# Performance work log

Measured on AMD Instinct MI355X. Metric: run time of the kernel, lower is better.

Reference implementation:

```python
import jax, jax.numpy as jnp
import numpy as np

B, C, H, W = 4, 64, 64, 64
CQK = C // 8


def setup_inputs() -> dict:
    key = jax.random.key(0)
    k0, k1, k2, k3, k4 = jax.random.split(key, 5)
    x = jax.random.normal(k0, (B, C, H, W), dtype=jnp.float32)
    # Conv1d kernel_size=1, bias=False -> plain [out, in] matmul weights
    Wq = jax.random.normal(k1, (CQK, C), dtype=jnp.float32) * 0.05
    Wk = jax.random.normal(k2, (CQK, C), dtype=jnp.float32) * 0.05
    Wv = jax.random.normal(k3, (C, C), dtype=jnp.float32) * 0.05
    # torch init is 0; use a nonzero scalar so the attention path is exercised
    gamma = jax.random.uniform(k4, (1,), dtype=jnp.float32)
    return {"x": x, "Wq": Wq, "Wk": Wk, "Wv": Wv, "gamma": gamma}


def reference(x, Wq, Wk, Wv, gamma):
    shape = x.shape                      # [B, C, H, W]
    xf = x.reshape(shape[0], shape[1], -1)  # [B, C, N]
    q = jnp.einsum('oc,bcn->bon', Wq, xf)   # [B, C/8, N]
    k = jnp.einsum('oc,bcn->bon', Wk, xf)   # [B, C/8, N]
    v = jnp.einsum('oc,bcn->bon', Wv, xf)   # [B, C, N]
    # score[b, n, m] = sum_c q[b, c, n] * k[b, c, m]  (no 1/sqrt(d) scale)
    score = jnp.einsum('bcn,bcm->bnm', q, k)  # [B, N, N]
    # unconventional softmax over dim=1 (rows/first N axis, i.e. per-column)
    score = jax.nn.softmax(score, axis=1)
    out = jnp.einsum('bcn,bnm->bcm', v, score)  # [B, C, N]
    attention = gamma * out + xf
    return attention.reshape(shape)
```

## Files before the change

kernel.cpp:

```cpp
#include <hip/hip_runtime.h>

#define BB 4
#define NN 4096

typedef __attribute__((ext_vector_type(8))) short short8v;
typedef __attribute__((ext_vector_type(4))) short short4v;
typedef __attribute__((ext_vector_type(4))) float float4v;

__device__ __forceinline__ unsigned short f2bf_rn(float f) {
    unsigned u = __float_as_uint(f);
    u += 0x7FFFu + ((u >> 16) & 1u);
    return (unsigned short)(u >> 16);
}

__global__ __launch_bounds__(256) void qkv_kernel(
    const float* __restrict__ x,
    const float* __restrict__ Wq, const float* __restrict__ Wk,
    const float* __restrict__ Wv,
    unsigned short* __restrict__ Qt, unsigned short* __restrict__ Kt,
    unsigned short* __restrict__ Vsw)
{
    __shared__ unsigned short xs[64][68];
    __shared__ unsigned short Ot[64][72];

    const int t    = threadIdx.x;
    const int w    = t >> 6;
    const int lane = t & 63;
    const int quad = lane >> 4;
    const int l15  = lane & 15;
    const int b    = blockIdx.y;
    const int n0   = blockIdx.x * 64;

    #pragma unroll
    for (int i = 0; i < 4; ++i) {
        int c  = (t >> 4) + i * 16;
        int n4 = (t & 15) * 4;
        float4 xv = *(const float4*)&x[(size_t)(b * 64 + c) * NN + n0 + n4];
        short4v pk;
        pk[0] = (short)f2bf_rn(xv.x); pk[1] = (short)f2bf_rn(xv.y);
        pk[2] = (short)f2bf_rn(xv.z); pk[3] = (short)f2bf_rn(xv.w);
        *(short4v*)&xs[c][n4] = pk;
    }

    short8v bw[5][2];
    #pragma unroll
    for (int ot = 0; ot < 5; ++ot) {
        int o = ot * 16 + l15;
        const float* base = (o < 8)  ? (Wq + o * 64)
                           : (o < 16) ? (Wk + (o - 8) * 64)
                                      : (Wv + (o - 16) * 64);
        #pragma unroll
        for (int h = 0; h < 2; ++h) {
            float4 u0 = *(const float4*)&base[h * 32 + quad * 8];
            float4 u1 = *(const float4*)&base[h * 32 + quad * 8 + 4];
            short8v f;
            f[0] = (short)f2bf_rn(u0.x); f[1] = (short)f2bf_rn(u0.y);
            f[2] = (short)f2bf_rn(u0.z); f[3] = (short)f2bf_rn(u0.w);
            f[4] = (short)f2bf_rn(u1.x); f[5] = (short)f2bf_rn(u1.y);
            f[6] = (short)f2bf_rn(u1.z); f[7] = (short)f2bf_rn(u1.w);
            bw[ot][h] = f;
        }
    }
    __syncthreads();

    short8v a0, a1;
    {
        unsigned short* p0 = (unsigned short*)&a0;
        unsigned short* p1 = (unsigned short*)&a1;
        const int nn = w * 16 + l15;
        #pragma unroll
        for (int j = 0; j < 8; ++j) {
            p0[j] = xs[quad * 8 + j][nn];
            p1[j] = xs[32 + quad * 8 + j][nn];
        }
    }

    const float4v zacc = {0.f, 0.f, 0.f, 0.f};
    #pragma unroll
    for (int ot = 0; ot < 5; ++ot) {
        float4v d = __builtin_amdgcn_mfma_f32_16x16x32_bf16(a0, bw[ot][0], zacc, 0, 0, 0);
        d = __builtin_amdgcn_mfma_f32_16x16x32_bf16(a1, bw[ot][1], d, 0, 0, 0);
        if (ot == 0) {
            #pragma unroll
            for (int r = 0; r < 4; ++r) {
                unsigned short v = f2bf_rn(d[r]);
                size_t n = (size_t)(n0 + w * 16 + quad * 4 + r);
                if (l15 < 8) Qt[((size_t)b * NN + n) * 8 + l15] = v;
                else         Kt[((size_t)b * NN + n) * 8 + (l15 - 8)] = v;
            }
        } else {
            short4v pk;
            #pragma unroll
            for (int r = 0; r < 4; ++r) pk[r] = (short)f2bf_rn(d[r]);
            *(short4v*)&Ot[(ot - 1) * 16 + l15][w * 16 + quad * 4] = pk;
        }
    }
    __syncthreads();

    {
        int ci = t >> 5, s = t & 31;
        int ct = ci >> 1, nbl = ci & 1;
        size_t nb = (size_t)blockIdx.x * 2 + nbl;
        unsigned short* cb = Vsw + ((size_t)(b * 4 + ct) * 128 + nb) * 512;
        #pragma unroll
        for (int h = 0; h < 2; ++h) {
            int l = s * 2 + h;
            short8v d = *(short8v*)&Ot[ct * 16 + (l & 15)][nbl * 32 + ((l >> 4) << 3)];
            *(short8v*)(cb + l * 8) = d;
        }
    }
}

__global__ __launch_bounds__(256, 4) void attn_kernel(
    const unsigned short* __restrict__ Qt,
    const unsigned short* __restrict__ Kt,
    const unsigned short* __restrict__ Vsw,
    const float* __restrict__ x, const float* __restrict__ gamma,
    float* __restrict__ out)
{
    __shared__ __align__(16) unsigned short Pb[4][16][40];
    __shared__ float Ored[4][64][17];
    __shared__ float Lred[4][16];
    __shared__ float Lf[16];

    const int t    = threadIdx.x;
    const int w    = t >> 6;
    const int lane = t & 63;
    const int quad = lane >> 4;
    const int l15  = lane & 15;
    const int b    = blockIdx.y;
    const int m0   = blockIdx.x * 16;

    const short8v zfrag = {0, 0, 0, 0, 0, 0, 0, 0};
    const float4v zacc  = {0.f, 0.f, 0.f, 0.f};

    short8v bk = zfrag;
    if (quad == 0)
        bk = *(const short8v*)(Kt + (size_t)(b * NN + m0 + l15) * 8);

    float4v acc[4];
    #pragma unroll
    for (int ct = 0; ct < 4; ++ct) acc[ct] = zacc;
    float Lacc = 0.f;

    const unsigned short* qrow = Qt + (size_t)(b * NN + w * 1024 + l15) * 8;
    const unsigned short* vptr = Vsw + ((size_t)b * 4 * 128 + w * 32) * 512 + lane * 8;

    short8v aq0n = zfrag, aq1n = zfrag;
    if (quad == 0) {
        aq0n = *(const short8v*)(qrow);
        aq1n = *(const short8v*)(qrow + 16 * 8);
    }
    short8v av0n = *(const short8v*)(vptr);
    short8v av1n = *(const short8v*)(vptr + 1 * 128 * 512);
    short8v av2n = *(const short8v*)(vptr + 2 * 128 * 512);
    short8v av3n = *(const short8v*)(vptr + 3 * 128 * 512);

    for (int it = 0; it < 32; ++it) {
        short8v aq0 = aq0n, aq1 = aq1n;
        short8v av0 = av0n, av1 = av1n, av2 = av2n, av3 = av3n;

        const int itn = (it + 1) & 31;
        av0n = *(const short8v*)(vptr + itn * 512);
        av1n = *(const short8v*)(vptr + 1 * 128 * 512 + itn * 512);
        av2n = *(const short8v*)(vptr + 2 * 128 * 512 + itn * 512);
        av3n = *(const short8v*)(vptr + 3 * 128 * 512 + itn * 512);
        if (quad == 0) {
            aq0n = *(const short8v*)(qrow + (size_t)(itn * 32) * 8);
            aq1n = *(const short8v*)(qrow + (size_t)(itn * 32 + 16) * 8);
        }

        float4v s0 = __builtin_amdgcn_mfma_f32_16x16x32_bf16(aq0, bk, zacc, 0, 0, 0);
        float4v s1 = __builtin_amdgcn_mfma_f32_16x16x32_bf16(aq1, bk, zacc, 0, 0, 0);

        float p[8];
        #pragma unroll
        for (int j = 0; j < 4; ++j) p[j]     = __expf(s0[j]);
        #pragma unroll
        for (int j = 0; j < 4; ++j) p[4 + j] = __expf(s1[j]);
        float ps = 0.f;
        #pragma unroll
        for (int j = 0; j < 8; ++j) ps += p[j];
        Lacc += ps;

        short4v pk0, pk1;
        #pragma unroll
        for (int j = 0; j < 4; ++j) {
            pk0[j] = (short)f2bf_rn(p[j]);
            pk1[j] = (short)f2bf_rn(p[4 + j]);
        }
        *(short4v*)&Pb[w][l15][quad * 4]      = pk0;
        *(short4v*)&Pb[w][l15][16 + quad * 4] = pk1;

        short8v bp = *(const short8v*)&Pb[w][l15][quad * 8];

        acc[0] = __builtin_amdgcn_mfma_f32_16x16x32_bf16(av0, bp, acc[0], 0, 0, 0);
        acc[1] = __builtin_amdgcn_mfma_f32_16x16x32_bf16(av1, bp, acc[1], 0, 0, 0);
        acc[2] = __builtin_amdgcn_mfma_f32_16x16x32_bf16(av2, bp, acc[2], 0, 0, 0);
        acc[3] = __builtin_amdgcn_mfma_f32_16x16x32_bf16(av3, bp, acc[3], 0, 0, 0);
    }

    Lacc += __shfl_xor(Lacc, 16, 64);
    Lacc += __shfl_xor(Lacc, 32, 64);
    if (lane < 16) Lred[w][lane] = Lacc;

    #pragma unroll
    for (int ct = 0; ct < 4; ++ct)
        #pragma unroll
        for (int r = 0; r < 4; ++r)
            Ored[w][ct * 16 + quad * 4 + r][l15] = acc[ct][r];
    __syncthreads();

    if (t < 16)
        Lf[t] = 1.f / (Lred[0][t] + Lred[1][t] + Lred[2][t] + Lred[3][t]);
    __syncthreads();

    {
        const float gv = gamma[0];
        int c = t >> 2, m4 = (t & 3) * 4;
        float4 o;
        #pragma unroll
        for (int i = 0; i < 4; ++i) {
            float s = Ored[0][c][m4 + i] + Ored[1][c][m4 + i]
                    + Ored[2][c][m4 + i] + Ored[3][c][m4 + i];
            ((float*)&o)[i] = s * Lf[m4 + i];
        }
        size_t gbase = (size_t)(b * 64 + c) * NN + m0 + m4;
        float4 xv = *(const float4*)&x[gbase];
        float4 r;
        r.x = gv * o.x + xv.x; r.y = gv * o.y + xv.y;
        r.z = gv * o.z + xv.z; r.w = gv * o.w + xv.w;
        *(float4*)&out[gbase] = r;
    }
}

extern "C" void kernel_launch(void* const* d_in, const int* in_sizes, int n_in,
                              void* d_out, int out_size, void* d_ws, size_t ws_size,
                              hipStream_t stream) {
    const float* x     = (const float*)d_in[0];
    const float* Wq    = (const float*)d_in[1];
    const float* Wk    = (const float*)d_in[2];
    const float* Wv    = (const float*)d_in[3];
    const float* gamma = (const float*)d_in[4];
    float* out = (float*)d_out;

    unsigned short* ws = (unsigned short*)d_ws;
    unsigned short* Qt  = ws;
    unsigned short* Kt  = Qt + (size_t)BB * NN * 8;
    unsigned short* Vsw = Kt + (size_t)BB * NN * 8;

    qkv_kernel<<<dim3(NN / 64, BB), 256, 0, stream>>>(x, Wq, Wk, Wv, Qt, Kt, Vsw);
    attn_kernel<<<dim3(NN / 16, BB), 256, 0, stream>>>(Qt, Kt, Vsw, x, gamma, out);
}
```

Baseline: 96.47 us.

## Software-pipeline attention loop with double-buffered P and fp32 FMA QKV projection

The attention loop is restructured so the score/exp/pack stage for the next key tile runs while the PV MFMAs consume the previous tile's P from a double-buffered LDS slot, with a prologue and epilogue. The QKV projection kernel replaces its bf16 MFMA path with fp32 FMA over LDS-staged x and transposed weights, and writes Q/K through LDS as coalesced 16-byte rows. The aim is to hide exp and LDS latency behind the matrix ops, and to improve Q/K store coalescing and projection precision. The cost is more LDS use in both kernels and more scalar FMA work in the projection.

New measurement: 97.10 us. About the same (+0.7%).

```diff
diff --git a/kernel.cpp b/kernel.cpp
--- a/kernel.cpp
+++ b/kernel.cpp
@@ -20,82 +20,71 @@
     unsigned short* __restrict__ Qt, unsigned short* __restrict__ Kt,
     unsigned short* __restrict__ Vsw)
 {
-    __shared__ unsigned short xs[64][68];
-    __shared__ unsigned short Ot[64][72];
-
-    const int t    = threadIdx.x;
-    const int w    = t >> 6;
-    const int lane = t & 63;
-    const int quad = lane >> 4;
-    const int l15  = lane & 15;
-    const int b    = blockIdx.y;
-    const int n0   = blockIdx.x * 64;
-
+    __shared__ float xs[64][68];
+    __shared__ float wl[64][81];
+    __shared__ unsigned short Ot[80][72];
+
+    const int t  = threadIdx.x;
+    const int b  = blockIdx.y;
+    const int n0 = blockIdx.x * 64;
+
+    #pragma unroll
+    for (int i = 0; i < 20; ++i) {
+        int idx = t + 256 * i;
+        int r = idx >> 6, c = idx & 63;
+        float w;
+        if (r < 8)       w = Wq[r * 64 + c];
+        else if (r < 16) w = Wk[(r - 8) * 64 + c];
+        else             w = Wv[(r - 16) * 64 + c];
+        wl[c][r] = w;
+    }
     #pragma unroll
     for (int i = 0; i < 4; ++i) {
-        int c  = (t >> 4) + i * 16;
-        int n4 = (t & 15) * 4;
-        float4 xv = *(const float4*)&x[(size_t)(b * 64 + c) * NN + n0 + n4];
+        int idx = t + 256 * i;
+        int c = idx >> 4, n4 = (idx & 15) * 4;
+        *(float4*)&xs[c][n4] = *(const float4*)&x[(size_t)(b * 64 + c) * NN + n0 + n4];
+    }
+    __syncthreads();
+
+    const int n4 = (t & 15) * 4;
+    const int og = t >> 4;
+
+    float acc[5][4];
+    #pragma unroll
+    for (int k = 0; k < 5; ++k)
+        #pragma unroll
+        for (int i = 0; i < 4; ++i) acc[k][i] = 0.f;
+
+    for (int c = 0; c < 64; ++c) {
+        float4 xv = *(const float4*)&xs[c][n4];
+        #pragma unroll
+        for (int k = 0; k < 5; ++k) {
+            float wv = wl[c][og * 5 + k];
+            acc[k][0] += wv * xv.x;
+            acc[k][1] += wv * xv.y;
+            acc[k][2] += wv * xv.z;
+            acc[k][3] += wv * xv.w;
+        }
+    }
+
+    #pragma unroll
+    for (int k = 0; k < 5; ++k) {
         short4v pk;
-        pk[0] = (short)f2bf_rn(xv.x); pk[1] = (short)f2bf_rn(xv.y);
-        pk[2] = (short)f2bf_rn(xv.z); pk[3] = (short)f2bf_rn(xv.w);
-        *(short4v*)&xs[c][n4] = pk;
-    }
-
-    short8v bw[5][2];
-    #pragma unroll
-    for (int ot = 0; ot < 5; ++ot) {
-        int o = ot * 16 + l15;
-        const float* base = (o < 8)  ? (Wq + o * 64)
-                           : (o < 16) ? (Wk + (o - 8) * 64)
-                                      : (Wv + (o - 16) * 64);
-        #pragma unroll
-        for (int h = 0; h < 2; ++h) {
-            float4 u0 = *(const float4*)&base[h * 32 + quad * 8];
-            float4 u1 = *(const float4*)&base[h * 32 + quad * 8 + 4];
-            short8v f;
-            f[0] = (short)f2bf_rn(u0.x); f[1] = (short)f2bf_rn(u0.y);
-            f[2] = (short)f2bf_rn(u0.z); f[3] = (short)f2bf_rn(u0.w);
-            f[4] = (short)f2bf_rn(u1.x); f[5] = (short)f2bf_rn(u1.y);
-            f[6] = (short)f2bf_rn(u1.z); f[7] = (short)f2bf_rn(u1.w);
-            bw[ot][h] = f;
-        }
-    }
-    __syncthreads();
-
-    short8v a0, a1;
-    {
-        unsigned short* p0 = (unsigned short*)&a0;
-        unsigned short* p1 = (unsigned short*)&a1;
-        const int nn = w * 16 + l15;
-        #pragma unroll
-        for (int j = 0; j < 8; ++j) {
-            p0[j] = xs[quad * 8 + j][nn];
-            p1[j] = xs[32 + quad * 8 + j][nn];
-        }
-    }
-
-    const float4v zacc = {0.f, 0.f, 0.f, 0.f};
-    #pragma unroll
-    for (int ot = 0; ot < 5; ++ot) {
-        float4v d = __builtin_amdgcn_mfma_f32_16x16x32_bf16(a0, bw[ot][0], zacc, 0, 0, 0);
-        d = __builtin_amdgcn_mfma_f32_16x16x32_bf16(a1, bw[ot][1], d, 0, 0, 0);
-        if (ot == 0) {
-            #pragma unroll
-            for (int r = 0; r < 4; ++r) {
-                unsigned short v = f2bf_rn(d[r]);
-                size_t n = (size_t)(n0 + w * 16 + quad * 4 + r);
-                if (l15 < 8) Qt[((size_t)b * NN + n) * 8 + l15] = v;
-                else         Kt[((size_t)b * NN + n) * 8 + (l15 - 8)] = v;
-            }
-        } else {
-            short4v pk;
-            #pragma unroll
-            for (int r = 0; r < 4; ++r) pk[r] = (short)f2bf_rn(d[r]);
-            *(short4v*)&Ot[(ot - 1) * 16 + l15][w * 16 + quad * 4] = pk;
-        }
-    }
-    __syncthreads();
+        #pragma unroll
+        for (int i = 0; i < 4; ++i) pk[i] = (short)f2bf_rn(acc[k][i]);
+        *(short4v*)&Ot[og * 5 + k][n4] = pk;
+    }
+    __syncthreads();
+
+    if (t < 128) {
+        int n = t & 63;
+        int rbase = (t < 64) ? 0 : 8;
+        short8v p;
+        #pragma unroll
+        for (int j = 0; j < 8; ++j) p[j] = (short)Ot[rbase + j][n];
+        unsigned short* dst = ((t < 64) ? Qt : Kt) + ((size_t)b * NN + n0 + n) * 8;
+        *(short8v*)dst = p;
+    }
 
     {
         int ci = t >> 5, s = t & 31;
@@ -105,7 +94,7 @@
         #pragma unroll
         for (int h = 0; h < 2; ++h) {
             int l = s * 2 + h;
-            short8v d = *(short8v*)&Ot[ct * 16 + (l & 15)][nbl * 32 + ((l >> 4) << 3)];
+            short8v d = *(short8v*)&Ot[16 + ct * 16 + (l & 15)][nbl * 32 + ((l >> 4) << 3)];
             *(short8v*)(cb + l * 8) = d;
         }
     }
@@ -118,7 +107,7 @@
     const float* __restrict__ x, const float* __restrict__ gamma,
     float* __restrict__ out)
 {
-    __shared__ __align__(16) unsigned short Pb[4][16][40];
+    __shared__ __align__(16) unsigned short Pb[4][2][16][40];
     __shared__ float Ored[4][64][17];
     __shared__ float Lred[4][16];
     __shared__ float Lf[16];
@@ -146,54 +135,77 @@
     const unsigned short* qrow = Qt + (size_t)(b * NN + w * 1024 + l15) * 8;
     const unsigned short* vptr = Vsw + ((size_t)b * 4 * 128 + w * 32) * 512 + lane * 8;
 
-    short8v aq0n = zfrag, aq1n = zfrag;
-    if (quad == 0) {
-        aq0n = *(const short8v*)(qrow);
-        aq1n = *(const short8v*)(qrow + 16 * 8);
-    }
-    short8v av0n = *(const short8v*)(vptr);
-    short8v av1n = *(const short8v*)(vptr + 1 * 128 * 512);
-    short8v av2n = *(const short8v*)(vptr + 2 * 128 * 512);
-    short8v av3n = *(const short8v*)(vptr + 3 * 128 * 512);
-
-    for (int it = 0; it < 32; ++it) {
-        short8v aq0 = aq0n, aq1 = aq1n;
-        short8v av0 = av0n, av1 = av1n, av2 = av2n, av3 = av3n;
-
-        const int itn = (it + 1) & 31;
-        av0n = *(const short8v*)(vptr + itn * 512);
-        av1n = *(const short8v*)(vptr + 1 * 128 * 512 + itn * 512);
-        av2n = *(const short8v*)(vptr + 2 * 128 * 512 + itn * 512);
-        av3n = *(const short8v*)(vptr + 3 * 128 * 512 + itn * 512);
+    short8v av0 = *(const short8v*)(vptr);
+    short8v av1 = *(const short8v*)(vptr + 1 * 128 * 512);
+    short8v av2 = *(const short8v*)(vptr + 2 * 128 * 512);
+    short8v av3 = *(const short8v*)(vptr + 3 * 128 * 512);
+    {
+        short8v aq0 = zfrag, aq1 = zfrag;
         if (quad == 0) {
-            aq0n = *(const short8v*)(qrow + (size_t)(itn * 32) * 8);
-            aq1n = *(const short8v*)(qrow + (size_t)(itn * 32 + 16) * 8);
-        }
-
+            aq0 = *(const short8v*)(qrow);
+            aq1 = *(const short8v*)(qrow + 16 * 8);
+        }
         float4v s0 = __builtin_amdgcn_mfma_f32_16x16x32_bf16(aq0, bk, zacc, 0, 0, 0);
         float4v s1 = __builtin_amdgcn_mfma_f32_16x16x32_bf16(aq1, bk, zacc, 0, 0, 0);
-
         float p[8];
         #pragma unroll
         for (int j = 0; j < 4; ++j) p[j]     = __expf(s0[j]);
         #pragma unroll
         for (int j = 0; j < 4; ++j) p[4 + j] = __expf(s1[j]);
-        float ps = 0.f;
-        #pragma unroll
-        for (int j = 0; j < 8; ++j) ps += p[j];
-        Lacc += ps;
-
+        #pragma unroll
+        for (int j = 0; j < 8; ++j) Lacc += p[j];
         short4v pk0, pk1;
         #pragma unroll
         for (int j = 0; j < 4; ++j) {
             pk0[j] = (short)f2bf_rn(p[j]);
             pk1[j] = (short)f2bf_rn(p[4 + j]);
         }
-        *(short4v*)&Pb[w][l15][quad * 4]      = pk0;
-        *(short4v*)&Pb[w][l15][16 + quad * 4] = pk1;
-
-        short8v bp = *(const short8v*)&Pb[w][l15][quad * 8];
-
+        *(short4v*)&Pb[w][0][l15][quad * 4]      = pk0;
+        *(short4v*)&Pb[w][0][l15][16 + quad * 4] = pk1;
+    }
+
+    for (int it = 0; it < 31; ++it) {
+        const int itn = it + 1;
+
+        short8v avn0 = *(const short8v*)(vptr + itn * 512);
+        short8v avn1 = *(const short8v*)(vptr + 1 * 128 * 512 + itn * 512);
+        short8v avn2 = *(const short8v*)(vptr + 2 * 128 * 512 + itn * 512);
+        short8v avn3 = *(const short8v*)(vptr + 3 * 128 * 512 + itn * 512);
+
+        short8v aq0 = zfrag, aq1 = zfrag;
+        if (quad == 0) {
+            aq0 = *(const short8v*)(qrow + (size_t)(itn * 32) * 8);
+            aq1 = *(const short8v*)(qrow + (size_t)(itn * 32 + 16) * 8);
+        }
+        float4v s0 = __builtin_amdgcn_mfma_f32_16x16x32_bf16(aq0, bk, zacc, 0, 0, 0);
+        float4v s1 = __builtin_amdgcn_mfma_f32_16x16x32_bf16(aq1, bk, zacc, 0, 0, 0);
+        float p[8];
+        #pragma unroll
+        for (int j = 0; j < 4; ++j) p[j]     = __expf(s0[j]);
+        #pragma unroll
+        for (int j = 0; j < 4; ++j) p[4 + j] = __expf(s1[j]);
+        #pragma unroll
+        for (int j = 0; j < 8; ++j) Lacc += p[j];
+        short4v pk0, pk1;
+        #pragma unroll
+        for (int j = 0; j < 4; ++j) {
+            pk0[j] = (short)f2bf_rn(p[j]);
+            pk1[j] = (short)f2bf_rn(p[4 + j]);
+        }
+        *(short4v*)&Pb[w][itn & 1][l15][quad * 4]      = pk0;
+        *(short4v*)&Pb[w][itn & 1][l15][16 + quad * 4] = pk1;
+
+        short8v bp = *(const short8v*)&Pb[w][it & 1][l15][quad * 8];
+        acc[0] = __builtin_amdgcn_mfma_f32_16x16x32_bf16(av0, bp, acc[0], 0, 0, 0);
+        acc[1] = __builtin_amdgcn_mfma_f32_16x16x32_bf16(av1, bp, acc[1], 0, 0, 0);
+        acc[2] = __builtin_amdgcn_mfma_f32_16x16x32_bf16(av2, bp, acc[2], 0, 0, 0);
+        acc[3] = __builtin_amdgcn_mfma_f32_16x16x32_bf16(av3, bp, acc[3], 0, 0, 0);
+
+        av0 = avn0; av1 = avn1; av2 = avn2; av3 = avn3;
+    }
+
+    {
+        short8v bp = *(const short8v*)&Pb[w][1][l15][quad * 8];
         acc[0] = __builtin_amdgcn_mfma_f32_16x16x32_bf16(av0, bp, acc[0], 0, 0, 0);
         acc[1] = __builtin_amdgcn_mfma_f32_16x16x32_bf16(av1, bp, acc[1], 0, 0, 0);
         acc[2] = __builtin_amdgcn_mfma_f32_16x16x32_bf16(av2, bp, acc[2], 0, 0, 0);
```
